# Kernel optimization log

Hardware: AMD Instinct MI355X
Metric: run time of the kernel (lower is better)

The kernel has to match this reference:

```python
import jax, jax.numpy as jnp
import numpy as np

ADAPT_STEP = 32


def setup_inputs() -> dict:
    key = jax.random.key(0)
    k1, k2, k3 = jax.random.split(key, 3)
    B, T, NB = 1024, 2048, 32
    x = jax.random.normal(k1, (B, T, NB), dtype=jnp.float32)
    quant_bins = jax.random.normal(k2, (NB,), dtype=jnp.float32)
    change_scales = jax.random.uniform(k3, (NB, 1), dtype=jnp.float32, minval=0.9, maxval=1.1)
    return {"x": x, "quant_bins": quant_bins, "change_scales": change_scales}


def reference(x, quant_bins, change_scales):
    B, T, NB = x.shape
    nchunks = T // ADAPT_STEP
    # (nchunks, B, ADAPT_STEP, NB) for lax.scan over chunks
    xs = x.reshape(B, nchunks, ADAPT_STEP, NB).transpose(1, 0, 2, 3)

    pred0 = jnp.zeros((B, 1), dtype=x.dtype)
    bins0 = jnp.broadcast_to(quant_bins[None, :], (B, NB))

    def step(carry, quant):
        pred, bins = carry                              # (B,1), (B,NB)
        d = jnp.einsum('bsn,bn->bs', quant, bins)       # per-step dequantized deltas
        out = pred + d                                  # (B, ADAPT_STEP)
        new_pred = pred + jnp.mean(d, axis=1, keepdims=True)
        symbol_probs = jnp.sum(quant, axis=1) / ADAPT_STEP  # (B, NB)
        scale = symbol_probs @ change_scales            # (B, 1)
        new_bins = bins * scale                         # adaptive bin rescale
        return (new_pred, new_bins), out

    _, outs = jax.lax.scan(step, (pred0, bins0), xs)    # outs: (nchunks, B, ADAPT_STEP)
    return outs.transpose(1, 0, 2).reshape(B, T)
```

## Files before the change

kernel.cpp:

```cpp
#include <hip/hip_runtime.h>


#define TLEN 2048
#define NB 32
#define NCHUNK 64

__global__ __launch_bounds__(256, 4) void delta_dequant_kernel(
    const float* __restrict__ x,
    const float* __restrict__ quant_bins,
    const float* __restrict__ change_scales,
    float* __restrict__ out)
{
    __shared__ float s_db[TLEN];
    __shared__ float s_dc[TLEN];
    __shared__ float s_S[NCHUNK];
    __shared__ float s_P[NCHUNK];

    const int b    = blockIdx.x;
    const int tid  = threadIdx.x;
    const int lane = tid & 63;
    const int wid  = tid >> 6;
    const int sub  = lane & 7;
    const int tg   = lane >> 3;

    const float4 qb4 = ((const float4*)quant_bins)[sub];
    const float4 cs4 = ((const float4*)change_scales)[sub];

    const float* __restrict__ xb = x + (size_t)b * (TLEN * NB);

    for (int k = 0; k < TLEN / 32; ++k) {
        int t = ((k * 4 + wid) << 3) + tg;
        float4 v = ((const float4*)(xb + t * NB))[sub];
        float db = v.x * qb4.x + v.y * qb4.y + v.z * qb4.z + v.w * qb4.w;
        float dc = v.x * cs4.x + v.y * cs4.y + v.z * cs4.z + v.w * cs4.w;
        db += __shfl_xor(db, 1); dc += __shfl_xor(dc, 1);
        db += __shfl_xor(db, 2); dc += __shfl_xor(dc, 2);
        db += __shfl_xor(db, 4); dc += __shfl_xor(dc, 4);
        if (sub == 0) { s_db[t] = db; s_dc[t] = dc; }
    }
    __syncthreads();

    float pa = 0.f, pg = 0.f;
    #pragma unroll
    for (int j = 0; j < 8; ++j) {
        pa += s_db[tid * 8 + j];
        pg += s_dc[tid * 8 + j];
    }
    pa += __shfl_xor(pa, 1); pg += __shfl_xor(pg, 1);
    pa += __shfl_xor(pa, 2); pg += __shfl_xor(pg, 2);
    if ((tid & 3) == 0) {
        s_P[tid >> 2] = pa * (1.0f / 32.0f);
        s_S[tid >> 2] = pg * (1.0f / 32.0f);
    }
    __syncthreads();

    if (tid == 0) {
        float S = 1.0f, pred = 0.0f;
        for (int c = 0; c < NCHUNK; ++c) {
            float G = s_S[c], A = s_P[c];
            s_S[c] = S; s_P[c] = pred;
            pred += S * A;
            S *= G;
        }
    }
    __syncthreads();

    float* __restrict__ ob = out + (size_t)b * TLEN;
    #pragma unroll
    for (int i = 0; i < 2; ++i) {
        int t4 = tid + i * 256;
        int c  = t4 >> 3;
        float S = s_S[c], P = s_P[c];
        float4 d4 = ((const float4*)s_db)[t4];
        float4 o;
        o.x = P + S * d4.x;
        o.y = P + S * d4.y;
        o.z = P + S * d4.z;
        o.w = P + S * d4.w;
        ((float4*)ob)[t4] = o;
    }
}

extern "C" void kernel_launch(void* const* d_in, const int* in_sizes, int n_in,
                              void* d_out, int out_size, void* d_ws, size_t ws_size,
                              hipStream_t stream) {
    const float* x  = (const float*)d_in[0];
    const float* qb = (const float*)d_in[1];
    const float* cs = (const float*)d_in[2];
    float* out = (float*)d_out;
    int B = out_size / TLEN;
    delta_dequant_kernel<<<B, 256, 0, stream>>>(x, qb, cs, out);
}
```

Baseline: 363.1 us.

## Use 512 threads per block and batch four independent loads per iteration

Doubles the block size to 512 threads (8 waves) and restructures the main loop so each thread issues four float4 loads before reducing them, raising memory-level parallelism. The chunk-sum and output phases are remapped to one float4 per thread. The aim is to hide HBM latency in a bandwidth-bound kernel, at the cost of more registers per thread and possible occupancy limits from the launch bounds.

```diff
diff --git a/kernel.cpp b/kernel.cpp
--- a/kernel.cpp
+++ b/kernel.cpp
@@ -5,7 +5,7 @@
 #define NB 32
 #define NCHUNK 64
 
-__global__ __launch_bounds__(256, 4) void delta_dequant_kernel(
+__global__ __launch_bounds__(512, 8) void delta_dequant_kernel(
     const float* __restrict__ x,
     const float* __restrict__ quant_bins,
     const float* __restrict__ change_scales,
@@ -28,29 +28,36 @@
 
     const float* __restrict__ xb = x + (size_t)b * (TLEN * NB);
 
-    for (int k = 0; k < TLEN / 32; ++k) {
-        int t = ((k * 4 + wid) << 3) + tg;
-        float4 v = ((const float4*)(xb + t * NB))[sub];
-        float db = v.x * qb4.x + v.y * qb4.y + v.z * qb4.z + v.w * qb4.w;
-        float dc = v.x * cs4.x + v.y * cs4.y + v.z * cs4.z + v.w * cs4.w;
-        db += __shfl_xor(db, 1); dc += __shfl_xor(dc, 1);
-        db += __shfl_xor(db, 2); dc += __shfl_xor(dc, 2);
-        db += __shfl_xor(db, 4); dc += __shfl_xor(dc, 4);
-        if (sub == 0) { s_db[t] = db; s_dc[t] = dc; }
+    for (int k = 0; k < 32; k += 4) {
+        const int tbase = k * 64 + wid * 8 + tg;
+        float4 v[4];
+        #pragma unroll
+        for (int u = 0; u < 4; ++u)
+            v[u] = ((const float4*)(xb + (size_t)(tbase + u * 64) * NB))[sub];
+        #pragma unroll
+        for (int u = 0; u < 4; ++u) {
+            float db = v[u].x * qb4.x + v[u].y * qb4.y + v[u].z * qb4.z + v[u].w * qb4.w;
+            float dc = v[u].x * cs4.x + v[u].y * cs4.y + v[u].z * cs4.z + v[u].w * cs4.w;
+            db += __shfl_xor(db, 1); dc += __shfl_xor(dc, 1);
+            db += __shfl_xor(db, 2); dc += __shfl_xor(dc, 2);
+            db += __shfl_xor(db, 4); dc += __shfl_xor(dc, 4);
+            if (sub == 0) { s_db[tbase + u * 64] = db; s_dc[tbase + u * 64] = dc; }
+        }
     }
     __syncthreads();
 
-    float pa = 0.f, pg = 0.f;
-    #pragma unroll
-    for (int j = 0; j < 8; ++j) {
-        pa += s_db[tid * 8 + j];
-        pg += s_dc[tid * 8 + j];
-    }
-    pa += __shfl_xor(pa, 1); pg += __shfl_xor(pg, 1);
-    pa += __shfl_xor(pa, 2); pg += __shfl_xor(pg, 2);
-    if ((tid & 3) == 0) {
-        s_P[tid >> 2] = pa * (1.0f / 32.0f);
-        s_S[tid >> 2] = pg * (1.0f / 32.0f);
+    {
+        float4 a4 = ((const float4*)s_db)[tid];
+        float4 g4 = ((const float4*)s_dc)[tid];
+        float pa = a4.x + a4.y + a4.z + a4.w;
+        float pg = g4.x + g4.y + g4.z + g4.w;
+        pa += __shfl_xor(pa, 1); pg += __shfl_xor(pg, 1);
+        pa += __shfl_xor(pa, 2); pg += __shfl_xor(pg, 2);
+        pa += __shfl_xor(pa, 4); pg += __shfl_xor(pg, 4);
+        if ((tid & 7) == 0) {
+            s_P[tid >> 3] = pa * (1.0f / 32.0f);
+            s_S[tid >> 3] = pg * (1.0f / 32.0f);
+        }
     }
     __syncthreads();
 
@@ -65,19 +72,17 @@
     }
     __syncthreads();
 
-    float* __restrict__ ob = out + (size_t)b * TLEN;
-    #pragma unroll
-    for (int i = 0; i < 2; ++i) {
-        int t4 = tid + i * 256;
-        int c  = t4 >> 3;
-        float S = s_S[c], P = s_P[c];
-        float4 d4 = ((const float4*)s_db)[t4];
+    {
+        float* __restrict__ ob = out + (size_t)b * TLEN;
+        const int c = tid >> 3;
+        const float S = s_S[c], P = s_P[c];
+        float4 d4 = ((const float4*)s_db)[tid];
         float4 o;
         o.x = P + S * d4.x;
         o.y = P + S * d4.y;
         o.z = P + S * d4.z;
         o.w = P + S * d4.w;
-        ((float4*)ob)[t4] = o;
+        ((float4*)ob)[tid] = o;
     }
 }
 
@@ -89,5 +94,5 @@
     const float* cs = (const float*)d_in[2];
     float* out = (float*)d_out;
     int B = out_size / TLEN;
-    delta_dequant_kernel<<<B, 256, 0, stream>>>(x, qb, cs, out);
+    delta_dequant_kernel<<<B, 512, 0, stream>>>(x, qb, cs, out);
 }
```

Result: no change. 361.1 us (-0.6%).
